# Performance work log

Measured on AMD Instinct MI355X. Metric: run time of the kernel, lower is better.

The kernel has to match this reference:

```python
import jax, jax.numpy as jnp
import numpy as np

B, S, IN_DIM, HID = 8, 2048, 1024, 1024


def setup_inputs() -> dict:
    key = jax.random.key(0)
    k1, k2, k3, k4, k5 = jax.random.split(key, 5)
    vec = jax.random.normal(k1, (B, S, IN_DIM), dtype=jnp.float32)
    # nn.Linear-style init scale
    wq_w = jax.random.normal(k2, (HID, IN_DIM), dtype=jnp.float32) / np.sqrt(IN_DIM)
    wq_b = jax.random.normal(k3, (HID,), dtype=jnp.float32) * 0.02
    lin_w = jax.random.normal(k4, (1, HID), dtype=jnp.float32) / np.sqrt(HID)
    lin_b = jax.random.normal(k5, (1,), dtype=jnp.float32) * 0.02
    return {"vec": vec, "wq_w": wq_w, "wq_b": wq_b, "lin_w": lin_w, "lin_b": lin_b}


def reference(vec, wq_w, wq_b, lin_w, lin_b):
    # NOTE: the original forward applies self.wq to BOTH q and k (wk/nq/nk unused).
    q = jnp.einsum('bsi,hi->bsh', vec, wq_w) + wq_b          # [B,S,H]
    ret = jnp.einsum('bsx,bsy->bxy', q, q)                    # [B,H,H] bilinear
    ret = jax.nn.relu(ret)
    out = jnp.einsum('bxy,y->bx', ret, lin_w[0]) + lin_b[0]   # Linear(H,1) -> [B,H]
    return out
```

## Files before the change

kernel.cpp:

```cpp
#include <hip/hip_runtime.h>


typedef short     bf16x8 __attribute__((ext_vector_type(8)));
typedef unsigned short u16x8 __attribute__((ext_vector_type(8)));
typedef float     f32x4 __attribute__((ext_vector_type(4)));
typedef long long i64;

#define FENCE asm volatile("" ::: "memory")
#define BARR  do { FENCE; __builtin_amdgcn_s_barrier(); FENCE; } while (0)
#define VMCNT(N) asm volatile("s_waitcnt vmcnt(" #N ")" ::: "memory")

__device__ inline unsigned short f2bf(float f) {
  unsigned int u = __float_as_uint(f);
  u += 0x7fffu + ((u >> 16) & 1u);
  return (unsigned short)(u >> 16);
}

__device__ inline u16x8 pack8(float4 a, float4 b) {
  u16x8 r;
  r[0] = f2bf(a.x); r[1] = f2bf(a.y); r[2] = f2bf(a.z); r[3] = f2bf(a.w);
  r[4] = f2bf(b.x); r[5] = f2bf(b.y); r[6] = f2bf(b.z); r[7] = f2bf(b.w);
  return r;
}

__device__ inline unsigned char f2fp8(float v) {
  int pk = __builtin_amdgcn_cvt_pk_fp8_f32(v, v, 0, false);
  return (unsigned char)(pk & 0xff);
}

__device__ inline void async16(void* lds, const void* g) {
  __builtin_amdgcn_global_load_lds(
      (const __attribute__((address_space(1))) void*)g,
      (__attribute__((address_space(3))) void*)lds,
      16, 0, 0);
}

__global__ __launch_bounds__(256) void prep(
    const float* __restrict__ vec, unsigned short* __restrict__ vecbf,
    const float* __restrict__ wq,  unsigned short* __restrict__ wqbf,
    const float* __restrict__ lin_b, float* __restrict__ out)
{
  if (blockIdx.x < 8192) {
    const int c   = ((blockIdx.x & 7) << 10) + (blockIdx.x >> 3);
    const int gid = c * 256 + threadIdx.x;
    const float4* s = (const float4*)(vec + (size_t)gid * 8);
    float4 a = s[0], b = s[1];
    *(u16x8*)(vecbf + (size_t)gid * 8) = pack8(a, b);
    const int oid = blockIdx.x * 256 + threadIdx.x;
    if (oid < 8192) out[oid] = lin_b[0];
  } else {
    const int i = (blockIdx.x - 8192) * 256 + threadIdx.x;
    const float4* s = (const float4*)(wq + (size_t)i * 8);
    float4 a = s[0], b = s[1];
    *(u16x8*)(wqbf + (size_t)i * 8) = pack8(a, b);
  }
}

__global__ void init_out(float* __restrict__ out, const float* __restrict__ lin_b) {
  int i = blockIdx.x * 256 + threadIdx.x;
  if (i < 8192) out[i] = lin_b[0];
}

__global__ __launch_bounds__(512, 2) void gemm_q8p(
    const unsigned short* __restrict__ A, const unsigned short* __restrict__ Bm,
    const float* __restrict__ bias, unsigned char* __restrict__ qT8)
{
  __shared__ unsigned short As[2][256 * 64];
  __shared__ unsigned short Bs[2][256 * 64];

  const int bid = blockIdx.y * 64 + blockIdx.x;
  const int xcd = bid & 7;
  const int idx = bid >> 3;
  const int m0 = (idx & 3) * 256;
  const int n0 = (xcd * 8 + (idx >> 2)) * 256;

  const int t    = threadIdx.x;
  const int lane = t & 63;
  const int wave = t >> 6;
  const int wm2  = (wave >> 2) * 64;
  const int wn2  = (wave & 3) * 32;
  const int quad = lane >> 4;
  const int lrow = lane & 15;

  const int srow = t >> 3;
  const int gch  = (t & 7) ^ (srow & 7);
  const unsigned short* gA = A  + (size_t)(m0 + srow) * 1024 + gch * 8;
  const unsigned short* gB = Bm + (size_t)(n0 + srow) * 1024 + gch * 8;

#define STAGE_A(SLOT, H, KT) do { \
  _Pragma("unroll") for (int p = 0; p < 2; ++p) \
    async16(&As[SLOT][((H)*128 + p*64)*64 + t*8], \
            gA + (size_t)((H)*128 + p*64)*1024 + (KT)*64); \
} while (0)

#define STAGE_B(SLOT, H, KT) do { \
  _Pragma("unroll") for (int p = 0; p < 2; ++p) \
    async16(&Bs[SLOT][((H)*128 + p*64)*64 + t*8], \
            gB + (size_t)((H)*128 + p*64)*1024 + (KT)*64); \
} while (0)

#define LDA_HALF(S, MH) do { \
  _Pragma("unroll") for (int f = 0; f < 4; ++f) \
  _Pragma("unroll") for (int kk = 0; kk < 2; ++kk) \
    a_[f][kk] = *(const bf16x8*)&As[S][((MH)*128 + wm2 + f*16 + lrow)*64 + \
                                       (((kk*4 + quad) ^ (lrow & 7)) * 8)]; \
} while (0)

#define LDB_HALF(S, NH, BREG) do { \
  _Pragma("unroll") for (int g = 0; g < 2; ++g) \
  _Pragma("unroll") for (int kk = 0; kk < 2; ++kk) \
    BREG[g][kk] = *(const bf16x8*)&Bs[S][((NH)*128 + wn2 + g*16 + lrow)*64 + \
                                         (((kk*4 + quad) ^ (lrow & 7)) * 8)]; \
} while (0)

#define MFMAQ(MH, NH, BREG) do { \
  __builtin_amdgcn_s_setprio(1); \
  _Pragma("unroll") for (int kk = 0; kk < 2; ++kk) \
  _Pragma("unroll") for (int f = 0; f < 4; ++f) \
  _Pragma("unroll") for (int g = 0; g < 2; ++g) \
    acc[MH][f][NH][g] = __builtin_amdgcn_mfma_f32_16x16x32_bf16( \
        a_[f][kk], BREG[g][kk], acc[MH][f][NH][g], 0, 0, 0); \
  __builtin_amdgcn_s_setprio(0); \
} while (0)

  f32x4 acc[2][4][2][2];
#pragma unroll
  for (int i = 0; i < 2; ++i)
#pragma unroll
    for (int f = 0; f < 4; ++f)
#pragma unroll
      for (int j = 0; j < 2; ++j)
#pragma unroll
        for (int g = 0; g < 2; ++g) acc[i][f][j][g] = (f32x4){0.f, 0.f, 0.f, 0.f};

  bf16x8 a_[4][2], b0_[2][2], b1_[2][2];

  STAGE_A(0, 0, 0);
  STAGE_B(0, 0, 0);
  STAGE_B(0, 1, 0);
  STAGE_A(0, 1, 0);
  VMCNT(4);
  BARR;

#pragma unroll 1
  for (int kt = 0; kt < 15; ++kt) {
    const int s  = kt & 1;
    const int so = s ^ 1;

    LDA_HALF(s, 0);
    LDB_HALF(s, 0, b0_);
    STAGE_A(so, 0, kt + 1);
    VMCNT(4);
    BARR;
    MFMAQ(0, 0, b0_);
    BARR;

    LDB_HALF(s, 1, b1_);
    STAGE_B(so, 0, kt + 1);
    VMCNT(4);
    BARR;
    MFMAQ(0, 1, b1_);
    BARR;

    LDA_HALF(s, 1);
    STAGE_B(so, 1, kt + 1);
    VMCNT(4);
    BARR;
    MFMAQ(1, 0, b0_);
    BARR;

    STAGE_A(so, 1, kt + 1);
    VMCNT(4);
    BARR;
    MFMAQ(1, 1, b1_);
    BARR;
  }

  LDA_HALF(1, 0);
  LDB_HALF(1, 0, b0_);
  VMCNT(2);
  BARR;
  MFMAQ(0, 0, b0_);
  BARR;

  LDB_HALF(1, 1, b1_);
  VMCNT(0);
  BARR;
  MFMAQ(0, 1, b1_);
  BARR;

  LDA_HALF(1, 1);
  MFMAQ(1, 0, b0_);
  MFMAQ(1, 1, b1_);

#pragma unroll
  for (int mh = 0; mh < 2; ++mh)
#pragma unroll
    for (int f = 0; f < 4; ++f)
#pragma unroll
      for (int r = 0; r < 4; ++r) {
        const int m = m0 + mh * 128 + wm2 + f * 16 + quad * 4 + r;
        const float bv = bias[m];
        unsigned char* row = qT8 + (size_t)m * 16384 + n0;
#pragma unroll
        for (int nh = 0; nh < 2; ++nh)
#pragma unroll
          for (int g = 0; g < 2; ++g)
            row[nh * 128 + wn2 + g * 16 + lrow] = f2fp8(acc[mh][f][nh][g][r] + bv);
      }

#undef STAGE_A
#undef STAGE_B
#undef LDA_HALF
#undef LDB_HALF
#undef MFMAQ
}

__global__ __launch_bounds__(256) void gemm_q_fused(
    const float* __restrict__ Wq, const float* __restrict__ V,
    const float* __restrict__ bias, unsigned char* __restrict__ qT8)
{
  __shared__ unsigned short As[128 * 32];
  __shared__ unsigned short Bs[128 * 32];

  const int m0 = blockIdx.y * 128;
  const int n0 = blockIdx.x * 128;
  const int t    = threadIdx.x;
  const int lane = t & 63;
  const int wave = t >> 6;
  const int wm = (wave >> 1) * 64;
  const int wn = (wave & 1) * 64;
  const int quad = lane >> 4;
  const int lrow = lane & 15;

  const int sr = t >> 1;
  const int sc = (t & 1) << 4;
  const float* gA = Wq + (size_t)(m0 + sr) * 1024 + sc;
  const float* gB = V  + (size_t)(n0 + sr) * 1024 + sc;

  f32x4 acc[4][4];
#pragma unroll
  for (int i = 0; i < 4; ++i)
#pragma unroll
    for (int j = 0; j < 4; ++j) acc[i][j] = (f32x4){0.f, 0.f, 0.f, 0.f};

  for (int k0 = 0; k0 < 1024; k0 += 32) {
    const float4* a4 = (const float4*)(gA + k0);
    const float4* b4 = (const float4*)(gB + k0);
    float4 av0 = a4[0], av1 = a4[1], av2 = a4[2], av3 = a4[3];
    float4 bv0 = b4[0], bv1 = b4[1], bv2 = b4[2], bv3 = b4[3];
    *(u16x8*)&As[sr * 32 + sc]     = pack8(av0, av1);
    *(u16x8*)&As[sr * 32 + sc + 8] = pack8(av2, av3);
    *(u16x8*)&Bs[sr * 32 + sc]     = pack8(bv0, bv1);
    *(u16x8*)&Bs[sr * 32 + sc + 8] = pack8(bv2, bv3);
    __syncthreads();

    bf16x8 af[4], bfr[4];
#pragma unroll
    for (int i = 0; i < 4; ++i)
      af[i] = *(const bf16x8*)&As[(wm + i * 16 + lrow) * 32 + quad * 8];
#pragma unroll
    for (int j = 0; j < 4; ++j)
      bfr[j] = *(const bf16x8*)&Bs[(wn + j * 16 + lrow) * 32 + quad * 8];
#pragma unroll
    for (int i = 0; i < 4; ++i)
#pragma unroll
      for (int j = 0; j < 4; ++j)
        acc[i][j] = __builtin_amdgcn_mfma_f32_16x16x32_bf16(af[i], bfr[j], acc[i][j], 0, 0, 0);
    __syncthreads();
  }

#pragma unroll
  for (int i = 0; i < 4; ++i) {
    const int mb = m0 + wm + i * 16 + quad * 4;
#pragma unroll
    for (int r = 0; r < 4; ++r) {
      const float bv = bias[mb + r];
#pragma unroll
      for (int j = 0; j < 4; ++j) {
        const int n = n0 + wn + j * 16 + lrow;
        qT8[(size_t)(mb + r) * 16384 + n] = f2fp8(acc[i][j][r] + bv);
      }
    }
  }
}

__global__ __launch_bounds__(256) void syrk_half8(
    const unsigned char* __restrict__ qT8, const float* __restrict__ W,
    float* __restrict__ out)
{
  __shared__ unsigned char As[2][128 * 128];
  __shared__ unsigned char Bs[2][64 * 128];

  const int bb   = blockIdx.x & 7;
  const int id2  = blockIdx.x >> 3;
  const int pair = id2 >> 1;
  const int yh   = id2 & 1;
  int tx = 0;
  while ((tx + 1) * (tx + 2) / 2 <= pair) ++tx;
  const int ty = pair - tx * (tx + 1) / 2;
  const int x0 = tx * 128;
  const int y0 = ty * 128 + yh * 64;
  const bool diag = (tx == ty);

  const int t    = threadIdx.x;
  const int lane = t & 63;
  const int wave = t >> 6;
  const int wm = (wave >> 1) * 64;
  const int wn = (wave & 1) * 32;
  const int quad = lane >> 4;
  const int lrow = lane & 15;

  const int srow = t >> 3;
  const int g16  = (t & 7) ^ (srow & 7);
  const size_t cb = (size_t)bb * 2048 + g16 * 16;
  const unsigned char* gA = qT8 + (size_t)(x0 + srow) * 16384 + cb;
  const unsigned char* gB = qT8 + (size_t)(y0 + srow) * 16384 + cb;

#define SSTAGE(SLOT, KT) do { \
  _Pragma("unroll") for (int p = 0; p < 4; ++p) \
    async16(&As[SLOT][p * 4096 + t * 16], gA + (size_t)p * 32 * 16384 + (KT) * 128); \
  _Pragma("unroll") for (int p = 0; p < 2; ++p) \
    async16(&Bs[SLOT][p * 4096 + t * 16], gB + (size_t)p * 32 * 16384 + (KT) * 128); \
} while (0)

#define SYRK_COMPUTE(S) do { \
  _Pragma("unroll") for (int kk = 0; kk < 4; ++kk) { \
    const int c = kk * 4 + quad; \
    const int off = (((c >> 1) ^ (lrow & 7)) << 4) + (c & 1) * 8; \
    i64 af[4], bfr[2]; \
    _Pragma("unroll") for (int i = 0; i < 4; ++i) \
      af[i] = *(const i64*)&As[S][(wm + i * 16 + lrow) * 128 + off]; \
    _Pragma("unroll") for (int j = 0; j < 2; ++j) \
      bfr[j] = *(const i64*)&Bs[S][(wn + j * 16 + lrow) * 128 + off]; \
    _Pragma("unroll") for (int i = 0; i < 4; ++i) \
      _Pragma("unroll") for (int j = 0; j < 2; ++j) \
        acc[i][j] = __builtin_amdgcn_mfma_f32_16x16x32_fp8_fp8(af[i], bfr[j], acc[i][j], 0, 0, 0); \
  } \
} while (0)

  f32x4 acc[4][2];
#pragma unroll
  for (int i = 0; i < 4; ++i)
#pragma unroll
    for (int j = 0; j < 2; ++j) acc[i][j] = (f32x4){0.f, 0.f, 0.f, 0.f};

  SSTAGE(0, 0);

#pragma unroll 1
  for (int kt = 0; kt < 15; ++kt) {
    const int s = kt & 1;
    SSTAGE(s ^ 1, kt + 1);
    VMCNT(6);
    BARR;
    SYRK_COMPUTE(s);
    BARR;
  }

  VMCNT(0);
  BARR;
  SYRK_COMPUTE(1);

#undef SSTAGE
#undef SYRK_COMPUTE

  float* ob = out + bb * 1024;

  float wv[2];
#pragma unroll
  for (int j = 0; j < 2; ++j) wv[j] = W[y0 + wn + j * 16 + lrow];

#pragma unroll
  for (int i = 0; i < 4; ++i) {
#pragma unroll
    for (int r = 0; r < 4; ++r) {
      float p = 0.f;
#pragma unroll
      for (int j = 0; j < 2; ++j) {
        float v = acc[i][j][r];
        v = v > 0.f ? v : 0.f;
        p += v * wv[j];
      }
#pragma unroll
      for (int off = 1; off < 16; off <<= 1) p += __shfl_xor(p, off, 64);
      if (lrow == 0)
        atomicAdd(&ob[x0 + wm + i * 16 + quad * 4 + r], p);
    }
  }

  if (!diag) {
    float wx[4][4];
#pragma unroll
    for (int i = 0; i < 4; ++i)
#pragma unroll
      for (int r = 0; r < 4; ++r)
        wx[i][r] = W[x0 + wm + i * 16 + quad * 4 + r];

#pragma unroll
    for (int j = 0; j < 2; ++j) {
      float pc = 0.f;
#pragma unroll
      for (int i = 0; i < 4; ++i)
#pragma unroll
        for (int r = 0; r < 4; ++r) {
          float v = acc[i][j][r];
          v = v > 0.f ? v : 0.f;
          pc += v * wx[i][r];
        }
      pc += __shfl_xor(pc, 16, 64);
      pc += __shfl_xor(pc, 32, 64);
      if (quad == 0)
        atomicAdd(&ob[y0 + wn + j * 16 + lrow], pc);
    }
  }
}

extern "C" void kernel_launch(void* const* d_in, const int* in_sizes, int n_in,
                              void* d_out, int out_size, void* d_ws, size_t ws_size,
                              hipStream_t stream) {
  const float* vec   = (const float*)d_in[0];
  const float* wq_w  = (const float*)d_in[1];
  const float* wq_b  = (const float*)d_in[2];
  const float* lin_w = (const float*)d_in[3];
  const float* lin_b = (const float*)d_in[4];
  float* out = (float*)d_out;

  unsigned char* qT8 = (unsigned char*)d_ws;
  const size_t need = (size_t)(16 + 32 + 2) * 1024 * 1024;

  if (ws_size >= need) {
    unsigned short* vecbf = (unsigned short*)((char*)d_ws + (size_t)16 * 1024 * 1024);
    unsigned short* wqbf  = vecbf + (size_t)16 * 1024 * 1024;
    prep<<<dim3(8192 + 512), dim3(256), 0, stream>>>(vec, vecbf, wq_w, wqbf, lin_b, out);
    gemm_q8p<<<dim3(64, 4), dim3(512), 0, stream>>>(wqbf, vecbf, wq_b, qT8);
  } else {
    init_out<<<dim3(32), dim3(256), 0, stream>>>(out, lin_b);
    gemm_q_fused<<<dim3(128, 8), dim3(256), 0, stream>>>(wq_w, vec, wq_b, qT8);
  }
  syrk_half8<<<dim3(576), dim3(256), 0, stream>>>(qT8, lin_w, out);
}
```

Baseline: 164.5 us.

## Replace 256x256 ping-pong GEMM with simpler 256x128 double-buffered tile kernel

Swaps the 512-thread 256x256-tile projection GEMM, with its quarter-staged interleaved loads and MFMA phases, for a 256-thread kernel using 256x128 tiles and a K-step of 32. Each K-step stages the whole next tile at once and runs a single compute phase per wave over 128x64 outputs. This cuts barrier count and code complexity and doubles the grid to 512 blocks. In exchange it drops the XCD-aware block remap, halves the K depth per stage, and lowers data reuse per block.

Measured after the change: 166.2 us. Within noise of the previous version (+1.0%).

```diff
diff --git a/kernel.cpp b/kernel.cpp
--- a/kernel.cpp
+++ b/kernel.cpp
@@ -61,159 +61,89 @@
   if (i < 8192) out[i] = lin_b[0];
 }
 
-__global__ __launch_bounds__(512, 2) void gemm_q8p(
+__global__ __launch_bounds__(256, 2) void gemm_2b(
     const unsigned short* __restrict__ A, const unsigned short* __restrict__ Bm,
     const float* __restrict__ bias, unsigned char* __restrict__ qT8)
 {
-  __shared__ unsigned short As[2][256 * 64];
-  __shared__ unsigned short Bs[2][256 * 64];
-
-  const int bid = blockIdx.y * 64 + blockIdx.x;
-  const int xcd = bid & 7;
-  const int idx = bid >> 3;
-  const int m0 = (idx & 3) * 256;
-  const int n0 = (xcd * 8 + (idx >> 2)) * 256;
+  __shared__ unsigned short As[2][256 * 32];
+  __shared__ unsigned short Bs[2][128 * 32];
+
+  const int n0 = blockIdx.x * 128;
+  const int m0 = blockIdx.y * 256;
 
   const int t    = threadIdx.x;
   const int lane = t & 63;
   const int wave = t >> 6;
-  const int wm2  = (wave >> 2) * 64;
-  const int wn2  = (wave & 3) * 32;
+  const int wm   = (wave >> 1) * 128;
+  const int wn   = (wave & 1) * 64;
   const int quad = lane >> 4;
   const int lrow = lane & 15;
 
-  const int srow = t >> 3;
-  const int gch  = (t & 7) ^ (srow & 7);
+  const int srow = t >> 2;
+  const int gch  = (t & 3) ^ ((srow >> 1) & 3);
   const unsigned short* gA = A  + (size_t)(m0 + srow) * 1024 + gch * 8;
   const unsigned short* gB = Bm + (size_t)(n0 + srow) * 1024 + gch * 8;
 
-#define STAGE_A(SLOT, H, KT) do { \
+#define GSTAGE(SLOT, KT) do { \
+  _Pragma("unroll") for (int p = 0; p < 4; ++p) \
+    async16(&As[SLOT][p * 2048 + t * 8], gA + (size_t)p * 64 * 1024 + (KT) * 32); \
   _Pragma("unroll") for (int p = 0; p < 2; ++p) \
-    async16(&As[SLOT][((H)*128 + p*64)*64 + t*8], \
-            gA + (size_t)((H)*128 + p*64)*1024 + (KT)*64); \
+    async16(&Bs[SLOT][p * 2048 + t * 8], gB + (size_t)p * 64 * 1024 + (KT) * 32); \
 } while (0)
 
-#define STAGE_B(SLOT, H, KT) do { \
-  _Pragma("unroll") for (int p = 0; p < 2; ++p) \
-    async16(&Bs[SLOT][((H)*128 + p*64)*64 + t*8], \
-            gB + (size_t)((H)*128 + p*64)*1024 + (KT)*64); \
-} while (0)
-
-#define LDA_HALF(S, MH) do { \
-  _Pragma("unroll") for (int f = 0; f < 4; ++f) \
-  _Pragma("unroll") for (int kk = 0; kk < 2; ++kk) \
-    a_[f][kk] = *(const bf16x8*)&As[S][((MH)*128 + wm2 + f*16 + lrow)*64 + \
-                                       (((kk*4 + quad) ^ (lrow & 7)) * 8)]; \
-} while (0)
-
-#define LDB_HALF(S, NH, BREG) do { \
-  _Pragma("unroll") for (int g = 0; g < 2; ++g) \
-  _Pragma("unroll") for (int kk = 0; kk < 2; ++kk) \
-    BREG[g][kk] = *(const bf16x8*)&Bs[S][((NH)*128 + wn2 + g*16 + lrow)*64 + \
-                                         (((kk*4 + quad) ^ (lrow & 7)) * 8)]; \
-} while (0)
-
-#define MFMAQ(MH, NH, BREG) do { \
+#define GCOMPUTE(S) do { \
+  bf16x8 af[8], bfr[4]; \
+  _Pragma("unroll") for (int f = 0; f < 8; ++f) { \
+    const int r = wm + f * 16 + lrow; \
+    af[f] = *(const bf16x8*)&As[S][r * 32 + ((quad ^ ((r >> 1) & 3)) * 8)]; \
+  } \
+  _Pragma("unroll") for (int g = 0; g < 4; ++g) { \
+    const int r = wn + g * 16 + lrow; \
+    bfr[g] = *(const bf16x8*)&Bs[S][r * 32 + ((quad ^ ((r >> 1) & 3)) * 8)]; \
+  } \
   __builtin_amdgcn_s_setprio(1); \
-  _Pragma("unroll") for (int kk = 0; kk < 2; ++kk) \
-  _Pragma("unroll") for (int f = 0; f < 4; ++f) \
-  _Pragma("unroll") for (int g = 0; g < 2; ++g) \
-    acc[MH][f][NH][g] = __builtin_amdgcn_mfma_f32_16x16x32_bf16( \
-        a_[f][kk], BREG[g][kk], acc[MH][f][NH][g], 0, 0, 0); \
+  _Pragma("unroll") for (int f = 0; f < 8; ++f) \
+  _Pragma("unroll") for (int g = 0; g < 4; ++g) \
+    acc[f][g] = __builtin_amdgcn_mfma_f32_16x16x32_bf16(af[f], bfr[g], acc[f][g], 0, 0, 0); \
   __builtin_amdgcn_s_setprio(0); \
 } while (0)
 
-  f32x4 acc[2][4][2][2];
-#pragma unroll
-  for (int i = 0; i < 2; ++i)
-#pragma unroll
-    for (int f = 0; f < 4; ++f)
-#pragma unroll
-      for (int j = 0; j < 2; ++j)
-#pragma unroll
-        for (int g = 0; g < 2; ++g) acc[i][f][j][g] = (f32x4){0.f, 0.f, 0.f, 0.f};
-
-  bf16x8 a_[4][2], b0_[2][2], b1_[2][2];
-
-  STAGE_A(0, 0, 0);
-  STAGE_B(0, 0, 0);
-  STAGE_B(0, 1, 0);
-  STAGE_A(0, 1, 0);
-  VMCNT(4);
-  BARR;
+  f32x4 acc[8][4];
+#pragma unroll
+  for (int f = 0; f < 8; ++f)
+#pragma unroll
+    for (int g = 0; g < 4; ++g) acc[f][g] = (f32x4){0.f, 0.f, 0.f, 0.f};
+
+  GSTAGE(0, 0);
 
 #pragma unroll 1
-  for (int kt = 0; kt < 15; ++kt) {
-    const int s  = kt & 1;
-    const int so = s ^ 1;
-
-    LDA_HALF(s, 0);
-    LDB_HALF(s, 0, b0_);
-    STAGE_A(so, 0, kt + 1);
-    VMCNT(4);
+  for (int kt = 0; kt < 31; ++kt) {
+    const int s = kt & 1;
+    GSTAGE(s ^ 1, kt + 1);
+    VMCNT(6);
     BARR;
-    MFMAQ(0, 0, b0_);
+    GCOMPUTE(s);
     BARR;
-
-    LDB_HALF(s, 1, b1_);
-    STAGE_B(so, 0, kt + 1);
-    VMCNT(4);
-    BARR;
-    MFMAQ(0, 1, b1_);
-    BARR;
-
-    LDA_HALF(s, 1);
-    STAGE_B(so, 1, kt + 1);
-    VMCNT(4);
-    BARR;
-    MFMAQ(1, 0, b0_);
-    BARR;
-
-    STAGE_A(so, 1, kt + 1);
-    VMCNT(4);
-    BARR;
-    MFMAQ(1, 1, b1_);
-    BARR;
-  }
-
-  LDA_HALF(1, 0);
-  LDB_HALF(1, 0, b0_);
-  VMCNT(2);
-  BARR;
-  MFMAQ(0, 0, b0_);
-  BARR;
-
-  LDB_HALF(1, 1, b1_);
+  }
+
   VMCNT(0);
   BARR;
-  MFMAQ(0, 1, b1_);
-  BARR;
-
-  LDA_HALF(1, 1);
-  MFMAQ(1, 0, b0_);
-  MFMAQ(1, 1, b1_);
-
-#pragma unroll
-  for (int mh = 0; mh < 2; ++mh)
-#pragma unroll
-    for (int f = 0; f < 4; ++f)
-#pragma unroll
-      for (int r = 0; r < 4; ++r) {
-        const int m = m0 + mh * 128 + wm2 + f * 16 + quad * 4 + r;
-        const float bv = bias[m];
-        unsigned char* row = qT8 + (size_t)m * 16384 + n0;
-#pragma unroll
-        for (int nh = 0; nh < 2; ++nh)
-#pragma unroll
-          for (int g = 0; g < 2; ++g)
-            row[nh * 128 + wn2 + g * 16 + lrow] = f2fp8(acc[mh][f][nh][g][r] + bv);
-      }
-
-#undef STAGE_A
-#undef STAGE_B
-#undef LDA_HALF
-#undef LDB_HALF
-#undef MFMAQ
+  GCOMPUTE(1);
+
+#undef GSTAGE
+#undef GCOMPUTE
+
+#pragma unroll
+  for (int f = 0; f < 8; ++f)
+#pragma unroll
+    for (int r = 0; r < 4; ++r) {
+      const int m = m0 + wm + f * 16 + quad * 4 + r;
+      const float bv = bias[m];
+      unsigned char* row = qT8 + (size_t)m * 16384 + n0 + wn;
+#pragma unroll
+      for (int g = 0; g < 4; ++g)
+        row[g * 16 + lrow] = f2fp8(acc[f][g][r] + bv);
+    }
 }
 
 __global__ __launch_bounds__(256) void gemm_q_fused(
@@ -432,7 +362,7 @@
     unsigned short* vecbf = (unsigned short*)((char*)d_ws + (size_t)16 * 1024 * 1024);
     unsigned short* wqbf  = vecbf + (size_t)16 * 1024 * 1024;
     prep<<<dim3(8192 + 512), dim3(256), 0, stream>>>(vec, vecbf, wq_w, wqbf, lin_b, out);
-    gemm_q8p<<<dim3(64, 4), dim3(512), 0, stream>>>(wqbf, vecbf, wq_b, qT8);
+    gemm_2b<<<dim3(128, 4), dim3(256), 0, stream>>>(wqbf, vecbf, wq_b, qT8);
   } else {
     init_out<<<dim3(32), dim3(256), 0, stream>>>(out, lin_b);
     gemm_q_fused<<<dim3(128, 8), dim3(256), 0, stream>>>(wq_w, vec, wq_b, qT8);
```
